# Performance work log

Measured on AMD Instinct MI355X. Metric: run time of the kernel, lower is better.

The kernel has to match this reference:

```python
import jax, jax.numpy as jnp
from jax import lax
import numpy as np

B, T, DM = 4, 2048, 768
LYR, DI, N, DC, R = 2, 1536, 64, 4, 48  # layers, d_inner, d_state, d_conv, dt_rank
EPS = 1e-5


def _silu(x):
    return x * jax.nn.sigmoid(x)


def _layernorm(x, w, b):
    m = x.mean(-1, keepdims=True)
    v = ((x - m) ** 2).mean(-1, keepdims=True)
    return (x - m) * lax.rsqrt(v + EPS) * w + b


def _mamba(x, W_in, Wc, bc, W_x, W_dt, b_dt, a_log, Dp, W_out):
    # x: [B,T,DM]; standard Mamba block (mamba_ssm), bias-free in/out projections
    b, t, _ = x.shape
    d_inner = Dp.shape[0]
    n = a_log.shape[1]
    r = W_dt.shape[1]
    xz = jnp.einsum('btd,ed->bte', x, W_in)      # [B,T,2*DI]
    u, z = jnp.split(xz, 2, axis=-1)
    # causal depthwise conv along T
    u_c = lax.conv_general_dilated(u.transpose(0, 2, 1), Wc[:, None, :], (1,),
                                   [(DC - 1, 0)], dimension_numbers=('NCH', 'OIH', 'NCH'),
                                   feature_group_count=d_inner)
    u_c = _silu((u_c + bc[None, :, None]).transpose(0, 2, 1))  # [B,T,DI]
    proj = jnp.einsum('btd,ed->bte', u_c, W_x)   # [B,T,R+2N]
    dt, Bm, Cm = proj[..., :r], proj[..., r:r + n], proj[..., r + n:]
    delta = jax.nn.softplus(jnp.einsum('btr,dr->btd', dt, W_dt) + b_dt)  # [B,T,DI]
    A = -jnp.exp(a_log)                           # [DI,N]

    def step(h, inp):
        d_t, u_t, B_t, C_t = inp                 # [B,DI],[B,DI],[B,N],[B,N]
        h = h * jnp.exp(d_t[..., None] * A) + d_t[..., None] * B_t[:, None, :] * u_t[..., None]
        return h, jnp.einsum('bdn,bn->bd', h, C_t)

    h0 = jnp.zeros((b, d_inner, n), x.dtype)
    _, ys = lax.scan(step, h0, (delta.transpose(1, 0, 2), u_c.transpose(1, 0, 2),
                                Bm.transpose(1, 0, 2), Cm.transpose(1, 0, 2)))
    y = ys.transpose(1, 0, 2) + u_c * Dp         # [B,T,DI]
    y = y * _silu(z)
    return jnp.einsum('btd,od->bto', y, W_out)   # [B,T,DM]


def setup_inputs() -> dict:
    key = jax.random.key(0)
    ks = jax.random.split(key, 12)
    s = 0.02
    A0 = jnp.log(jnp.arange(1, N + 1, dtype=jnp.float32))  # standard S4D-real init
    return {
        'x': jax.random.normal(ks[0], (B, T, DM), jnp.float32),
        'mask': jnp.ones((B, T), jnp.float32),
        'film_gamma': 1.0 + 0.1 * jax.random.normal(ks[1], (LYR, B, T, DM), jnp.float32),
        'film_beta': 0.1 * jax.random.normal(ks[2], (LYR, B, T, DM), jnp.float32),
        'in_proj_w': s * jax.random.normal(ks[3], (LYR, 2 * DI, DM), jnp.float32),
        'conv_w': s * jax.random.normal(ks[4], (LYR, DI, DC), jnp.float32),
        'conv_b': s * jax.random.normal(ks[5], (LYR, DI), jnp.float32),
        'x_proj_w': s * jax.random.normal(ks[6], (LYR, R + 2 * N, DI), jnp.float32),
        'dt_proj_w': s * jax.random.normal(ks[7], (LYR, DI, R), jnp.float32),
        'dt_proj_b': jnp.full((LYR, DI), -4.6, jnp.float32),  # softplus -> dt ~ 0.01
        'A_log': jnp.broadcast_to(A0, (LYR, DI, N)).copy(),
        'D': jnp.ones((LYR, DI), jnp.float32),
        'out_proj_w': s * jax.random.normal(ks[8], (LYR, DM, DI), jnp.float32),
        'ln_w': jnp.ones((LYR, DM), jnp.float32),
        'ln_b': jnp.zeros((LYR, DM), jnp.float32),
    }


def reference(x, mask, film_gamma, film_beta, in_proj_w, conv_w, conv_b, x_proj_w,
              dt_proj_w, dt_proj_b, A_log, D, out_proj_w, ln_w, ln_b):
    x = x * mask[..., None]
    for i in range(in_proj_w.shape[0]):
        residual = x
        h = _mamba(x, in_proj_w[i], conv_w[i], conv_b[i], x_proj_w[i], dt_proj_w[i],
                   dt_proj_b[i], A_log[i], D[i], out_proj_w[i])
        h = _layernorm(h, ln_w[i], ln_b[i])
        h = film_gamma[i] * h + film_beta[i]
        x = h + residual  # dropout is identity in eval mode
    return x
```

## Files before the change

### kernel.cpp

```cpp
#include <hip/hip_runtime.h>
#include <hip/hip_bf16.h>
#include <math.h>

#define BBv   4
#define TTv   2048
#define DMv   768
#define DIv   1536
#define NSv   64
#define DCv   4
#define RRv   48
#define PJW   176
#define NLYR  2
#define MROWS (BBv * TTv)

#define TBLK  32
#define LDST  68

typedef __attribute__((ext_vector_type(8))) short short8;
typedef __attribute__((ext_vector_type(4))) float f32x4;

__device__ __forceinline__ __hip_bfloat16 f2bf(float f) { return __float2bfloat16(f); }
__device__ __forceinline__ float bf2f(__hip_bfloat16 h) { return __bfloat162float(h); }

__global__ void cvt_weights_kernel(const float* __restrict__ w_in,
                                   const float* __restrict__ w_xp,
                                   const float* __restrict__ w_dt,
                                   const float* __restrict__ w_out,
                                   __hip_bfloat16* __restrict__ o_in,
                                   __hip_bfloat16* __restrict__ o_xp,
                                   __hip_bfloat16* __restrict__ o_dt,
                                   __hip_bfloat16* __restrict__ o_out)
{
    const size_t S1 = (size_t)NLYR * 2 * DIv * DMv;
    const size_t S2 = (size_t)NLYR * PJW * DIv;
    const size_t S3 = (size_t)NLYR * DIv * RRv;
    const size_t S4 = (size_t)NLYR * DMv * DIv;
    const size_t total = S1 + S2 + S3 + S4;
    for (size_t i = (size_t)blockIdx.x * blockDim.x + threadIdx.x; i < total;
         i += (size_t)gridDim.x * blockDim.x) {
        if (i < S1)                o_in[i]            = f2bf(w_in[i]);
        else if (i < S1 + S2)      o_xp[i - S1]       = f2bf(w_xp[i - S1]);
        else if (i < S1 + S2 + S3) o_dt[i - S1 - S2]  = f2bf(w_dt[i - S1 - S2]);
        else                       o_out[i - S1 - S2 - S3] = f2bf(w_out[i - S1 - S2 - S3]);
    }
}

__global__ void mask_x_kernel(const float* __restrict__ x,
                              const float* __restrict__ mask,
                              float* __restrict__ x_cur,
                              __hip_bfloat16* __restrict__ x_bf)
{
    size_t idx = (size_t)blockIdx.x * 256 + threadIdx.x;
    if (idx >= (size_t)MROWS * DMv) return;
    size_t row = idx / DMv;
    float v = x[idx] * mask[row];
    x_cur[idx] = v;
    x_bf[idx] = f2bf(v);
}

template<int EPI>
__global__ __launch_bounds__(256)
void gemm_nt(const __hip_bfloat16* __restrict__ A, int lda,
             const __hip_bfloat16* __restrict__ Bw, int ldb,
             float* __restrict__ Cf, __hip_bfloat16* __restrict__ Ch, int ldc,
             const float* __restrict__ bias, int M, int N, int K)
{
    __shared__ __align__(16) __hip_bfloat16 sA[64 * 48];
    __shared__ __align__(16) __hip_bfloat16 sB[64 * 48];
    const int tid = threadIdx.x;
    const int m0 = blockIdx.y * 64;
    const int n0 = blockIdx.x * 64;
    const int w = tid >> 6, lane = tid & 63;
    const int wr = (w >> 1) << 5;
    const int wc = (w & 1) << 5;
    const int lr = lane & 15, lk = lane >> 4;
    const int srow = tid >> 2;
    const int scol = (tid & 3) << 3;
    f32x4 acc[2][2] = {};
    const bool bvalid = (n0 + srow) < N;

    for (int k0 = 0; k0 < K; k0 += 32) {
        uint4 av = {0u, 0u, 0u, 0u}, bv = {0u, 0u, 0u, 0u};
        const bool kv = (k0 + scol) < K;
        if (kv)
            av = *(const uint4*)(A + (size_t)(m0 + srow) * lda + (k0 + scol));
        if (kv && bvalid)
            bv = *(const uint4*)(Bw + (size_t)(n0 + srow) * ldb + (k0 + scol));
        *(uint4*)(sA + srow * 48 + scol) = av;
        *(uint4*)(sB + srow * 48 + scol) = bv;
        __syncthreads();
        short8 af0 = *(const short8*)(sA + (wr + lr) * 48 + (lk << 3));
        short8 af1 = *(const short8*)(sA + (wr + 16 + lr) * 48 + (lk << 3));
        short8 bf0 = *(const short8*)(sB + (wc + lr) * 48 + (lk << 3));
        short8 bf1 = *(const short8*)(sB + (wc + 16 + lr) * 48 + (lk << 3));
        acc[0][0] = __builtin_amdgcn_mfma_f32_16x16x32_bf16(af0, bf0, acc[0][0], 0, 0, 0);
        acc[0][1] = __builtin_amdgcn_mfma_f32_16x16x32_bf16(af0, bf1, acc[0][1], 0, 0, 0);
        acc[1][0] = __builtin_amdgcn_mfma_f32_16x16x32_bf16(af1, bf0, acc[1][0], 0, 0, 0);
        acc[1][1] = __builtin_amdgcn_mfma_f32_16x16x32_bf16(af1, bf1, acc[1][1], 0, 0, 0);
        __syncthreads();
    }
    #pragma unroll
    for (int i = 0; i < 2; ++i) {
        #pragma unroll
        for (int j = 0; j < 2; ++j) {
            const int col = n0 + wc + (j << 4) + lr;
            if (col >= N) continue;
            #pragma unroll
            for (int r = 0; r < 4; ++r) {
                const int row = m0 + wr + (i << 4) + (lk << 2) + r;
                float v = acc[i][j][r];
                if constexpr (EPI == 0) {
                    Cf[(size_t)row * ldc + col] = v;
                } else if constexpr (EPI == 1) {
                    Ch[(size_t)row * ldc + col] = f2bf(v);
                } else if constexpr (EPI == 2) {
                    float xx = v + bias[col];
                    Cf[(size_t)row * ldc + col] =
                        fmaxf(xx, 0.f) + log1pf(__expf(-fabsf(xx)));
                } else {
                    if (col < RRv)
                        Ch[(size_t)row * RRv + col] = f2bf(v);
                    else if (col < RRv + NSv)
                        Cf[(size_t)row * 128 + 2 * (col - RRv)] = v;
                    else
                        Cf[(size_t)row * 128 + 2 * (col - RRv - NSv) + 1] = v;
                }
            }
        }
    }
}

__global__ void conv_silu_kernel(const __hip_bfloat16* __restrict__ xz,
                                 const float* __restrict__ Wc,
                                 const float* __restrict__ bc,
                                 __hip_bfloat16* __restrict__ uc)
{
    size_t idx = (size_t)blockIdx.x * 256 + threadIdx.x;
    if (idx >= (size_t)MROWS * DIv) return;
    int d = (int)(idx % DIv);
    size_t row = idx / DIv;
    int t = (int)(row % TTv);
    float acc = bc[d];
    #pragma unroll
    for (int k = 0; k < DCv; ++k) {
        int tt = t - (DCv - 1) + k;
        if (tt >= 0)
            acc += Wc[d * DCv + k] *
                   bf2f(xz[(row - (DCv - 1) + k) * (2 * DIv) + d]);
    }
    float s = acc / (1.f + __expf(-acc));
    uc[idx] = f2bf(s);
}

__global__ __launch_bounds__(256, 4)
void scan_kernel(const float* __restrict__ delta,
                 const __hip_bfloat16* __restrict__ uc,
                 const __hip_bfloat16* __restrict__ xz,
                 const float* __restrict__ BC,
                 const float* __restrict__ a_log,
                 const float* __restrict__ Dp,
                 __hip_bfloat16* __restrict__ y)
{
    __shared__ __align__(16) float vbuf[4 * TBLK * LDST];
    const int w = threadIdx.x >> 6;
    const int lane = threadIdx.x & 63;
    const int wid = blockIdx.x * 4 + w;
    const int b = __builtin_amdgcn_readfirstlane(wid / DIv);
    const int d = __builtin_amdgcn_readfirstlane(wid % DIv);
    const size_t bT = (size_t)b * TTv;

    const float A2 = -__expf(a_log[(size_t)d * NSv + lane]) * 1.44269504088896f;
    const float Dd = Dp[d];

    const float* dp = delta + bT * DIv + d;
    const __hip_bfloat16* up = uc + bT * DIv + d;
    const float* bcp = BC + bT * 128 + 2 * lane;
    float* vb = vbuf + w * (TBLK * LDST);

    float2 bc[2][8];
    float  dl[2][8];
    float  uu[2][8];

    #pragma unroll
    for (int i = 0; i < 8; ++i) {
        bc[0][i] = *(const float2*)(bcp + (size_t)i * 128);
        dl[0][i] = dp[(size_t)i * DIv];
        uu[0][i] = bf2f(up[(size_t)i * DIv]);
    }

    float h = 0.f;
    for (int t0 = 0; t0 < TTv; t0 += TBLK) {
        #pragma unroll
        for (int q = 0; q < 4; ++q) {
            const int cur = q & 1, nxt = cur ^ 1;
            const int tn = t0 + q * 8 + 8;
            if (tn < TTv) {
                #pragma unroll
                for (int i = 0; i < 8; ++i) {
                    bc[nxt][i] = *(const float2*)(bcp + (size_t)(tn + i) * 128);
                    dl[nxt][i] = dp[(size_t)(tn + i) * DIv];
                    uu[nxt][i] = bf2f(up[(size_t)(tn + i) * DIv]);
                }
            }
            #pragma unroll
            for (int i = 0; i < 8; ++i) {
                const float dlt = dl[cur][i];
                const float e  = exp2f(dlt * A2);
                const float du = dlt * uu[cur][i];
                h = fmaf(h, e, du * bc[cur][i].x);
                vb[(q * 8 + i) * LDST + lane] = h * bc[cur][i].y;
            }
        }
        __asm__ volatile("s_waitcnt lgkmcnt(0)" ::: "memory");
        const int r = lane & 31;
        const int cbase = (lane >> 5) << 5;
        const float* vr = vb + r * LDST + cbase;
        f32x4 a = *(const f32x4*)(vr);
        #pragma unroll
        for (int k = 1; k < 8; ++k)
            a += *(const f32x4*)(vr + 4 * k);
        float s = a[0] + a[1] + a[2] + a[3];
        s += __shfl_xor(s, 32, 64);
        if (lane < 32) {
            const size_t rowg = bT + t0 + r;
            const float u = bf2f(uc[rowg * DIv + d]);
            const float z = bf2f(xz[rowg * 2 * DIv + DIv + d]);
            float yv = s + u * Dd;
            yv *= z / (1.f + __expf(-z));
            y[rowg * DIv + d] = f2bf(yv);
        }
    }
}

__global__ __launch_bounds__(256)
void ln_film_res_kernel(const float* __restrict__ h,
                        const float* __restrict__ xres,
                        const float* __restrict__ lw,
                        const float* __restrict__ lb,
                        const float* __restrict__ gamma,
                        const float* __restrict__ beta,
                        float* __restrict__ xout,
                        __hip_bfloat16* __restrict__ xbf)
{
    __shared__ float sm[4];
    const int row = blockIdx.x;
    const int tid = threadIdx.x;
    const int w = tid >> 6, lane = tid & 63;
    const float* hr = h + (size_t)row * DMv;
    float v0 = hr[tid], v1 = hr[tid + 256], v2 = hr[tid + 512];

    float s = v0 + v1 + v2;
    #pragma unroll
    for (int off = 32; off > 0; off >>= 1) s += __shfl_xor(s, off, 64);
    if (lane == 0) sm[w] = s;
    __syncthreads();
    float mean = (sm[0] + sm[1] + sm[2] + sm[3]) * (1.f / DMv);
    __syncthreads();

    float d0 = v0 - mean, d1 = v1 - mean, d2 = v2 - mean;
    float vs = d0 * d0 + d1 * d1 + d2 * d2;
    #pragma unroll
    for (int off = 32; off > 0; off >>= 1) vs += __shfl_xor(vs, off, 64);
    if (lane == 0) sm[w] = vs;
    __syncthreads();
    float var = (sm[0] + sm[1] + sm[2] + sm[3]) * (1.f / DMv);
    float rstd = rsqrtf(var + 1e-5f);

    const float dv[3] = {d0, d1, d2};
    #pragma unroll
    for (int e = 0; e < 3; ++e) {
        int c = tid + e * 256;
        size_t gi = (size_t)row * DMv + c;
        float ln = dv[e] * rstd * lw[c] + lb[c];
        float f = gamma[gi] * ln + beta[gi];
        float o = f + xres[gi];
        xout[gi] = o;
        xbf[gi] = f2bf(o);
    }
}

extern "C" void kernel_launch(void* const* d_in, const int* in_sizes, int n_in,
                              void* d_out, int out_size, void* d_ws, size_t ws_size,
                              hipStream_t stream)
{
    const float* x     = (const float*)d_in[0];
    const float* mask  = (const float*)d_in[1];
    const float* fg    = (const float*)d_in[2];
    const float* fb    = (const float*)d_in[3];
    const float* w_in  = (const float*)d_in[4];
    const float* w_c   = (const float*)d_in[5];
    const float* b_c   = (const float*)d_in[6];
    const float* w_xp  = (const float*)d_in[7];
    const float* w_dt  = (const float*)d_in[8];
    const float* b_dt  = (const float*)d_in[9];
    const float* a_log = (const float*)d_in[10];
    const float* Dp    = (const float*)d_in[11];
    const float* w_out = (const float*)d_in[12];
    const float* ln_w  = (const float*)d_in[13];
    const float* ln_b  = (const float*)d_in[14];

    char* p = (char*)d_ws;
    __hip_bfloat16* xz_bf  = (__hip_bfloat16*)p; p += (size_t)MROWS * 2 * DIv * 2;
    __hip_bfloat16* uc_bf  = (__hip_bfloat16*)p; p += (size_t)MROWS * DIv * 2;
    __hip_bfloat16* y_bf   = (__hip_bfloat16*)p; p += (size_t)MROWS * DIv * 2;
    __hip_bfloat16* x_bf   = (__hip_bfloat16*)p; p += (size_t)MROWS * DMv * 2;
    __hip_bfloat16* dtA_bf = (__hip_bfloat16*)p; p += (size_t)MROWS * RRv * 2;
    __hip_bfloat16* wbf_in = (__hip_bfloat16*)p; p += (size_t)NLYR * 2 * DIv * DMv * 2;
    __hip_bfloat16* wbf_xp = (__hip_bfloat16*)p; p += (size_t)NLYR * PJW * DIv * 2;
    __hip_bfloat16* wbf_dt = (__hip_bfloat16*)p; p += (size_t)NLYR * DIv * RRv * 2;
    __hip_bfloat16* wbf_out= (__hip_bfloat16*)p; p += (size_t)NLYR * DMv * DIv * 2;
    float* BCbuf = (float*)p; p += (size_t)MROWS * 128 * 4;
    float* delta = (float*)p; p += (size_t)MROWS * DIv * 4;
    float* x_cur = (float*)p; p += (size_t)MROWS * DMv * 4;
    float* hbuf  = delta;

    cvt_weights_kernel<<<4096, 256, 0, stream>>>(w_in, w_xp, w_dt, w_out,
                                                 wbf_in, wbf_xp, wbf_dt, wbf_out);
    mask_x_kernel<<<(MROWS * DMv) / 256, 256, 0, stream>>>(x, mask, x_cur, x_bf);

    for (int L = 0; L < NLYR; ++L) {
        const __hip_bfloat16* WinL  = wbf_in  + (size_t)L * 2 * DIv * DMv;
        const __hip_bfloat16* WxpL  = wbf_xp  + (size_t)L * PJW * DIv;
        const __hip_bfloat16* WdtL  = wbf_dt  + (size_t)L * DIv * RRv;
        const __hip_bfloat16* WoutL = wbf_out + (size_t)L * DMv * DIv;

        gemm_nt<1><<<dim3(2 * DIv / 64, MROWS / 64), 256, 0, stream>>>(
            x_bf, DMv, WinL, DMv, nullptr, xz_bf, 2 * DIv, nullptr,
            MROWS, 2 * DIv, DMv);

        conv_silu_kernel<<<(MROWS * DIv) / 256, 256, 0, stream>>>(
            xz_bf, w_c + (size_t)L * DIv * DCv, b_c + (size_t)L * DIv, uc_bf);

        gemm_nt<3><<<dim3((PJW + 63) / 64, MROWS / 64), 256, 0, stream>>>(
            uc_bf, DIv, WxpL, DIv, BCbuf, dtA_bf, 0, nullptr,
            MROWS, PJW, DIv);

        gemm_nt<2><<<dim3(DIv / 64, MROWS / 64), 256, 0, stream>>>(
            dtA_bf, RRv, WdtL, RRv, delta, nullptr, DIv,
            b_dt + (size_t)L * DIv, MROWS, DIv, RRv);

        scan_kernel<<<(BBv * DIv) / 4, 256, 0, stream>>>(
            delta, uc_bf, xz_bf, BCbuf,
            a_log + (size_t)L * DIv * NSv, Dp + (size_t)L * DIv, y_bf);

        gemm_nt<0><<<dim3(DMv / 64, MROWS / 64), 256, 0, stream>>>(
            y_bf, DIv, WoutL, DIv, hbuf, nullptr, DMv, nullptr,
            MROWS, DMv, DIv);

        float* xo = (L == NLYR - 1) ? (float*)d_out : x_cur;
        ln_film_res_kernel<<<MROWS, 256, 0, stream>>>(
            hbuf, x_cur, ln_w + (size_t)L * DMv, ln_b + (size_t)L * DMv,
            fg + (size_t)L * MROWS * DMv, fb + (size_t)L * MROWS * DMv,
            xo, x_bf);
    }
}
```

Baseline: 1.920 ms.

## Store scan inputs channel-major so the selective scan reads contiguous time series

The scan kernel previously read delta, u and z with a stride of DI (or 2*DI) per timestep. Those reads now come from transposed [DI, B*T] buffers: the in-projection epilogue writes z transposed, the dt-projection epilogue writes delta transposed, and explicit transpose kernels convert u_c before the scan and y after it. The scan time block drops from 32 to 16 and the occupancy hint rises to 6 waves, which shrinks register and LDS use. In exchange there are two extra transpose passes over the data and strided epilogue stores in the GEMMs.

```diff
diff --git a/kernel.cpp b/kernel.cpp
--- a/kernel.cpp
+++ b/kernel.cpp
@@ -13,7 +13,7 @@
 #define NLYR  2
 #define MROWS (BBv * TTv)
 
-#define TBLK  32
+#define TBLK  16
 #define LDST  68
 
 typedef __attribute__((ext_vector_type(8))) short short8;
@@ -58,11 +58,40 @@
     x_bf[idx] = f2bf(v);
 }
 
+__global__ __launch_bounds__(256)
+void transpose_bf16(const ushort* __restrict__ in, ushort* __restrict__ out,
+                    int R, int C)
+{
+    __shared__ ushort s[64][68];
+    const int tx = threadIdx.x & 15;
+    const int ty = threadIdx.x >> 4;
+    const size_t r0 = (size_t)blockIdx.y * 64;
+    const size_t c0 = (size_t)blockIdx.x * 64;
+    #pragma unroll
+    for (int i = 0; i < 4; ++i) {
+        int r = ty + 16 * i;
+        ushort4 v = *(const ushort4*)(in + (r0 + r) * C + c0 + tx * 4);
+        *(ushort4*)&s[r][tx * 4] = v;
+    }
+    __syncthreads();
+    #pragma unroll
+    for (int i = 0; i < 4; ++i) {
+        int c = ty + 16 * i;
+        ushort4 v;
+        v.x = s[tx * 4 + 0][c];
+        v.y = s[tx * 4 + 1][c];
+        v.z = s[tx * 4 + 2][c];
+        v.w = s[tx * 4 + 3][c];
+        *(ushort4*)(out + (c0 + c) * R + r0 + tx * 4) = v;
+    }
+}
+
 template<int EPI>
 __global__ __launch_bounds__(256)
 void gemm_nt(const __hip_bfloat16* __restrict__ A, int lda,
              const __hip_bfloat16* __restrict__ Bw, int ldb,
-             float* __restrict__ Cf, __hip_bfloat16* __restrict__ Ch, int ldc,
+             float* __restrict__ Cf, __hip_bfloat16* __restrict__ Ch,
+             __hip_bfloat16* __restrict__ ChT, int ldc,
              const float* __restrict__ bias, int M, int N, int K)
 {
     __shared__ __align__(16) __hip_bfloat16 sA[64 * 48];
@@ -104,20 +133,25 @@
         #pragma unroll
         for (int j = 0; j < 2; ++j) {
             const int col = n0 + wc + (j << 4) + lr;
+            const int rowb = m0 + wr + (i << 4) + (lk << 2);
             if (col >= N) continue;
-            #pragma unroll
-            for (int r = 0; r < 4; ++r) {
-                const int row = m0 + wr + (i << 4) + (lk << 2) + r;
-                float v = acc[i][j][r];
-                if constexpr (EPI == 0) {
-                    Cf[(size_t)row * ldc + col] = v;
-                } else if constexpr (EPI == 1) {
-                    Ch[(size_t)row * ldc + col] = f2bf(v);
-                } else if constexpr (EPI == 2) {
-                    float xx = v + bias[col];
-                    Cf[(size_t)row * ldc + col] =
-                        fmaxf(xx, 0.f) + log1pf(__expf(-fabsf(xx)));
-                } else {
+            if constexpr (EPI == 0) {
+                #pragma unroll
+                for (int r = 0; r < 4; ++r)
+                    Cf[(size_t)(rowb + r) * ldc + col] = acc[i][j][r];
+            } else if constexpr (EPI == 2) {
+                f32x4 sp;
+                #pragma unroll
+                for (int r = 0; r < 4; ++r) {
+                    float xx = acc[i][j][r] + bias[col];
+                    sp[r] = fmaxf(xx, 0.f) + log1pf(__expf(-fabsf(xx)));
+                }
+                *(f32x4*)(Cf + (size_t)col * MROWS + rowb) = sp;
+            } else if constexpr (EPI == 3) {
+                #pragma unroll
+                for (int r = 0; r < 4; ++r) {
+                    const int row = rowb + r;
+                    float v = acc[i][j][r];
                     if (col < RRv)
                         Ch[(size_t)row * RRv + col] = f2bf(v);
                     else if (col < RRv + NSv)
@@ -125,12 +159,23 @@
                     else
                         Cf[(size_t)row * 128 + 2 * (col - RRv - NSv) + 1] = v;
                 }
+            } else {
+                if (col < DIv) {
+                    #pragma unroll
+                    for (int r = 0; r < 4; ++r)
+                        Ch[(size_t)(rowb + r) * DIv + col] = f2bf(acc[i][j][r]);
+                } else {
+                    union { ushort4 v; __hip_bfloat16 h[4]; } zz;
+                    #pragma unroll
+                    for (int r = 0; r < 4; ++r) zz.h[r] = f2bf(acc[i][j][r]);
+                    *(ushort4*)(ChT + (size_t)(col - DIv) * MROWS + rowb) = zz.v;
+                }
             }
         }
     }
 }
 
-__global__ void conv_silu_kernel(const __hip_bfloat16* __restrict__ xz,
+__global__ void conv_silu_kernel(const __hip_bfloat16* __restrict__ u_raw,
                                  const float* __restrict__ Wc,
                                  const float* __restrict__ bc,
                                  __hip_bfloat16* __restrict__ uc)
@@ -146,20 +191,20 @@
         int tt = t - (DCv - 1) + k;
         if (tt >= 0)
             acc += Wc[d * DCv + k] *
-                   bf2f(xz[(row - (DCv - 1) + k) * (2 * DIv) + d]);
+                   bf2f(u_raw[(row - (DCv - 1) + k) * DIv + d]);
     }
     float s = acc / (1.f + __expf(-acc));
     uc[idx] = f2bf(s);
 }
 
-__global__ __launch_bounds__(256, 4)
-void scan_kernel(const float* __restrict__ delta,
-                 const __hip_bfloat16* __restrict__ uc,
-                 const __hip_bfloat16* __restrict__ xz,
+__global__ __launch_bounds__(256, 6)
+void scan_kernel(const float* __restrict__ deltaT,
+                 const __hip_bfloat16* __restrict__ ucT,
+                 const __hip_bfloat16* __restrict__ zT,
                  const float* __restrict__ BC,
                  const float* __restrict__ a_log,
                  const float* __restrict__ Dp,
-                 __hip_bfloat16* __restrict__ y)
+                 __hip_bfloat16* __restrict__ yT)
 {
     __shared__ __align__(16) float vbuf[4 * TBLK * LDST];
     const int w = threadIdx.x >> 6;
@@ -168,12 +213,13 @@
     const int b = __builtin_amdgcn_readfirstlane(wid / DIv);
     const int d = __builtin_amdgcn_readfirstlane(wid % DIv);
     const size_t bT = (size_t)b * TTv;
+    const size_t dbase = (size_t)d * MROWS + bT;
 
     const float A2 = -__expf(a_log[(size_t)d * NSv + lane]) * 1.44269504088896f;
     const float Dd = Dp[d];
 
-    const float* dp = delta + bT * DIv + d;
-    const __hip_bfloat16* up = uc + bT * DIv + d;
+    const float* dp = deltaT + dbase;
+    const __hip_bfloat16* up = ucT + dbase;
     const float* bcp = BC + bT * 128 + 2 * lane;
     float* vb = vbuf + w * (TBLK * LDST);
 
@@ -184,50 +230,49 @@
     #pragma unroll
     for (int i = 0; i < 8; ++i) {
         bc[0][i] = *(const float2*)(bcp + (size_t)i * 128);
-        dl[0][i] = dp[(size_t)i * DIv];
-        uu[0][i] = bf2f(up[(size_t)i * DIv]);
+        dl[0][i] = dp[i];
+        uu[0][i] = bf2f(up[i]);
     }
 
     float h = 0.f;
     for (int t0 = 0; t0 < TTv; t0 += TBLK) {
         #pragma unroll
-        for (int q = 0; q < 4; ++q) {
-            const int cur = q & 1, nxt = cur ^ 1;
+        for (int q = 0; q < 2; ++q) {
             const int tn = t0 + q * 8 + 8;
             if (tn < TTv) {
                 #pragma unroll
                 for (int i = 0; i < 8; ++i) {
-                    bc[nxt][i] = *(const float2*)(bcp + (size_t)(tn + i) * 128);
-                    dl[nxt][i] = dp[(size_t)(tn + i) * DIv];
-                    uu[nxt][i] = bf2f(up[(size_t)(tn + i) * DIv]);
+                    bc[q ^ 1][i] = *(const float2*)(bcp + (size_t)(tn + i) * 128);
+                    dl[q ^ 1][i] = dp[tn + i];
+                    uu[q ^ 1][i] = bf2f(up[tn + i]);
                 }
             }
             #pragma unroll
             for (int i = 0; i < 8; ++i) {
-                const float dlt = dl[cur][i];
-                const float e  = exp2f(dlt * A2);
-                const float du = dlt * uu[cur][i];
-                h = fmaf(h, e, du * bc[cur][i].x);
-                vb[(q * 8 + i) * LDST + lane] = h * bc[cur][i].y;
+                const float dlt = dl[q][i];
+                const float e = exp2f(dlt * A2);
+                h = fmaf(h, e, (dlt * uu[q][i]) * bc[q][i].x);
+                vb[(q * 8 + i) * LDST + lane] = h * bc[q][i].y;
             }
         }
         __asm__ volatile("s_waitcnt lgkmcnt(0)" ::: "memory");
-        const int r = lane & 31;
-        const int cbase = (lane >> 5) << 5;
-        const float* vr = vb + r * LDST + cbase;
+        const int r = lane & 15;
+        const int cb = (lane >> 4) << 4;
+        const float* vr = vb + r * LDST + cb;
         f32x4 a = *(const f32x4*)(vr);
-        #pragma unroll
-        for (int k = 1; k < 8; ++k)
-            a += *(const f32x4*)(vr + 4 * k);
+        a += *(const f32x4*)(vr + 4);
+        a += *(const f32x4*)(vr + 8);
+        a += *(const f32x4*)(vr + 12);
         float s = a[0] + a[1] + a[2] + a[3];
+        s += __shfl_xor(s, 16, 64);
         s += __shfl_xor(s, 32, 64);
-        if (lane < 32) {
-            const size_t rowg = bT + t0 + r;
-            const float u = bf2f(uc[rowg * DIv + d]);
-            const float z = bf2f(xz[rowg * 2 * DIv + DIv + d]);
+        if (lane < 16) {
+            const size_t g = dbase + t0 + r;
+            const float u = bf2f(ucT[g]);
+            const float z = bf2f(zT[g]);
             float yv = s + u * Dd;
             yv *= z / (1.f + __expf(-z));
-            y[rowg * DIv + d] = f2bf(yv);
+            yT[g] = f2bf(yv);
         }
     }
 }
@@ -300,19 +345,20 @@
     const float* ln_b  = (const float*)d_in[14];
 
     char* p = (char*)d_ws;
-    __hip_bfloat16* xz_bf  = (__hip_bfloat16*)p; p += (size_t)MROWS * 2 * DIv * 2;
-    __hip_bfloat16* uc_bf  = (__hip_bfloat16*)p; p += (size_t)MROWS * DIv * 2;
-    __hip_bfloat16* y_bf   = (__hip_bfloat16*)p; p += (size_t)MROWS * DIv * 2;
-    __hip_bfloat16* x_bf   = (__hip_bfloat16*)p; p += (size_t)MROWS * DMv * 2;
-    __hip_bfloat16* dtA_bf = (__hip_bfloat16*)p; p += (size_t)MROWS * RRv * 2;
-    __hip_bfloat16* wbf_in = (__hip_bfloat16*)p; p += (size_t)NLYR * 2 * DIv * DMv * 2;
-    __hip_bfloat16* wbf_xp = (__hip_bfloat16*)p; p += (size_t)NLYR * PJW * DIv * 2;
-    __hip_bfloat16* wbf_dt = (__hip_bfloat16*)p; p += (size_t)NLYR * DIv * RRv * 2;
-    __hip_bfloat16* wbf_out= (__hip_bfloat16*)p; p += (size_t)NLYR * DMv * DIv * 2;
-    float* BCbuf = (float*)p; p += (size_t)MROWS * 128 * 4;
-    float* delta = (float*)p; p += (size_t)MROWS * DIv * 4;
-    float* x_cur = (float*)p; p += (size_t)MROWS * DMv * 4;
-    float* hbuf  = delta;
+    __hip_bfloat16* uraw_yT = (__hip_bfloat16*)p; p += (size_t)MROWS * DIv * 2;
+    __hip_bfloat16* uc_y    = (__hip_bfloat16*)p; p += (size_t)MROWS * DIv * 2;
+    __hip_bfloat16* ucT     = (__hip_bfloat16*)p; p += (size_t)DIv * MROWS * 2;
+    __hip_bfloat16* zT      = (__hip_bfloat16*)p; p += (size_t)DIv * MROWS * 2;
+    __hip_bfloat16* x_bf    = (__hip_bfloat16*)p; p += (size_t)MROWS * DMv * 2;
+    __hip_bfloat16* dtA_bf  = (__hip_bfloat16*)p; p += (size_t)MROWS * RRv * 2;
+    __hip_bfloat16* wbf_in  = (__hip_bfloat16*)p; p += (size_t)NLYR * 2 * DIv * DMv * 2;
+    __hip_bfloat16* wbf_xp  = (__hip_bfloat16*)p; p += (size_t)NLYR * PJW * DIv * 2;
+    __hip_bfloat16* wbf_dt  = (__hip_bfloat16*)p; p += (size_t)NLYR * DIv * RRv * 2;
+    __hip_bfloat16* wbf_out = (__hip_bfloat16*)p; p += (size_t)NLYR * DMv * DIv * 2;
+    float* BCbuf  = (float*)p; p += (size_t)MROWS * 128 * 4;
+    float* deltaT = (float*)p; p += (size_t)DIv * MROWS * 4;
+    float* x_cur  = (float*)p; p += (size_t)MROWS * DMv * 4;
+    float* hbuf   = deltaT;
 
     cvt_weights_kernel<<<4096, 256, 0, stream>>>(w_in, w_xp, w_dt, w_out,
                                                  wbf_in, wbf_xp, wbf_dt, wbf_out);
@@ -324,27 +370,33 @@
         const __hip_bfloat16* WdtL  = wbf_dt  + (size_t)L * DIv * RRv;
         const __hip_bfloat16* WoutL = wbf_out + (size_t)L * DMv * DIv;
 
-        gemm_nt<1><<<dim3(2 * DIv / 64, MROWS / 64), 256, 0, stream>>>(
-            x_bf, DMv, WinL, DMv, nullptr, xz_bf, 2 * DIv, nullptr,
+        gemm_nt<4><<<dim3(2 * DIv / 64, MROWS / 64), 256, 0, stream>>>(
+            x_bf, DMv, WinL, DMv, nullptr, uraw_yT, zT, 0, nullptr,
             MROWS, 2 * DIv, DMv);
 
         conv_silu_kernel<<<(MROWS * DIv) / 256, 256, 0, stream>>>(
-            xz_bf, w_c + (size_t)L * DIv * DCv, b_c + (size_t)L * DIv, uc_bf);
+            uraw_yT, w_c + (size_t)L * DIv * DCv, b_c + (size_t)L * DIv, uc_y);
+
+        transpose_bf16<<<dim3(DIv / 64, MROWS / 64), 256, 0, stream>>>(
+            (const ushort*)uc_y, (ushort*)ucT, MROWS, DIv);
 
         gemm_nt<3><<<dim3((PJW + 63) / 64, MROWS / 64), 256, 0, stream>>>(
-            uc_bf, DIv, WxpL, DIv, BCbuf, dtA_bf, 0, nullptr,
+            uc_y, DIv, WxpL, DIv, BCbuf, dtA_bf, nullptr, 0, nullptr,
             MROWS, PJW, DIv);
 
         gemm_nt<2><<<dim3(DIv / 64, MROWS / 64), 256, 0, stream>>>(
-            dtA_bf, RRv, WdtL, RRv, delta, nullptr, DIv,
+            dtA_bf, RRv, WdtL, RRv, deltaT, nullptr, nullptr, 0,
             b_dt + (size_t)L * DIv, MROWS, DIv, RRv);
 
         scan_kernel<<<(BBv * DIv) / 4, 256, 0, stream>>>(
-            delta, uc_bf, xz_bf, BCbuf,
-            a_log + (size_t)L * DIv * NSv, Dp + (size_t)L * DIv, y_bf);
+            deltaT, ucT, zT, BCbuf,
+            a_log + (size_t)L * DIv * NSv, Dp + (size_t)L * DIv, uraw_yT);
+
+        transpose_bf16<<<dim3(MROWS / 64, DIv / 64), 256, 0, stream>>>(
+            (const ushort*)uraw_yT, (ushort*)uc_y, DIv, MROWS);
 
         gemm_nt<0><<<dim3(DMv / 64, MROWS / 64), 256, 0, stream>>>(
-            y_bf, DIv, WoutL, DIv, hbuf, nullptr, DMv, nullptr,
+            uc_y, DIv, WoutL, DIv, hbuf, nullptr, nullptr, DMv, nullptr,
             MROWS, DMv, DIv);
 
         float* xo = (L == NLYR - 1) ? (float*)d_out : x_cur;
```

New measurement: 1.660 ms. 13.6% less time.
